# Performance work log

Hardware: AMD Instinct MI355X
Metric: run time of the kernel (lower is better)

## Reference

```python
import jax, jax.numpy as jnp
import numpy as np

N = 500_000      # total observations
D = 40           # per-observation feature dim
S = 2048         # number of segments (time series)
WIDTH = 128      # psi hidden width
LATENT = 128     # latent width
DOT = 64         # dot_prod_dim
HEADS = 4        # n_heads


def setup_inputs() -> dict:
    key = jax.random.key(0)
    ks = jax.random.split(key, 12)

    def he(k, shape):
        fan_in = shape[0]
        lim = np.sqrt(6.0 / fan_in)
        return jax.random.uniform(k, shape, jnp.float32, -lim, lim)

    inputs = jax.random.normal(ks[0], (N, D), jnp.float32)
    segment_ids = jnp.sort(jax.random.randint(ks[1], (N,), 0, S))
    lengths = jax.random.randint(ks[2], (S,), 0, 300)
    return {
        "inputs": inputs,
        "segment_ids": segment_ids,
        "lengths": lengths,
        "W1": he(ks[3], (D, WIDTH)),      "b1": jnp.zeros((WIDTH,), jnp.float32),
        "W2": he(ks[4], (WIDTH, WIDTH)), "b2": jnp.zeros((WIDTH,), jnp.float32),
        "W3": he(ks[5], (WIDTH, LATENT)),"b3": jnp.zeros((LATENT,), jnp.float32),
        "Wr": he(ks[6], (LATENT, LATENT)),"br": jnp.zeros((LATENT,), jnp.float32),
        "W_k": he(ks[7], (LATENT + D, DOT * HEADS)),
        "W_q": jax.random.normal(ks[8], (HEADS, DOT), jnp.float32) * 0.02,
    }


def segment_softmax(x, seg, num_segments):
    # x: [N, H]; softmax over elements sharing the same segment id
    m = jax.ops.segment_max(x, seg, num_segments, indices_are_sorted=True)
    e = jnp.exp(x - m[seg])
    denom = jax.ops.segment_sum(e, seg, num_segments, indices_are_sorted=True)
    return e / denom[seg]


def reference(inputs, segment_ids, lengths, W1, b1, W2, b2, W3, b3, Wr, br, W_k, W_q):
    relu = jax.nn.relu
    # psi: 2 hidden dense layers + latent projection (all relu)
    h = relu(inputs @ W1 + b1)
    h = relu(h @ W2 + b2)
    enc = relu(h @ W3 + b3)                                   # [N, LATENT]
    # segment mean aggregation
    sums = jax.ops.segment_sum(enc, segment_ids, S, indices_are_sorted=True)
    counts = jax.ops.segment_sum(jnp.ones((enc.shape[0], 1), enc.dtype),
                                 segment_ids, S, indices_are_sorted=True)
    agg = sums / jnp.maximum(counts, 1.0)                      # [S, LATENT]
    agg = relu(agg @ Wr + br)                                  # rho
    # broadcast back and combine
    combined = jnp.concatenate([inputs, agg[segment_ids]], axis=-1)  # [N, D+LATENT]
    keys = (combined @ W_k).reshape(-1, HEADS, DOT)            # split+stack == reshape
    preattn = jnp.einsum('nhd,hd->nh', keys, W_q) / jnp.sqrt(jnp.float32(DOT))
    attn = segment_softmax(preattn, segment_ids, S)            # [N, H]
    # match original: list of per-head [N, 1] tensors -> stacked [H, N, 1]
    return jnp.transpose(attn)[..., None]
```

## Files before the change

### kernel.cpp

```cpp
#include <hip/hip_runtime.h>
#include <math.h>


#define NROWS 500000
#define DIM 40
#define NSEG 2048
#define DOTD 64
#define NH 4
#define BLOCK 256

__global__ __launch_bounds__(BLOCK) void prep0_kernel(
    const float* __restrict__ Wk,
    const float* __restrict__ Wq,
    float* __restrict__ denom,
    float* __restrict__ wxg)
{
    const int t = (int)(blockIdx.x * BLOCK + threadIdx.x);
    if (t < NSEG * NH) denom[t] = 0.f;
    if (blockIdx.x == 32 && threadIdx.x < DIM * NH) {
        const int d = (int)threadIdx.x >> 2;
        const int h = (int)threadIdx.x & 3;
        const float* wkp = Wk + d * (NH * DOTD) + h * DOTD;
        const float* wqp = Wq + h * DOTD;
        float acc = 0.f;
        #pragma unroll
        for (int j = 0; j < DOTD; ++j) acc += wkp[j] * wqp[j];
        wxg[threadIdx.x] = acc * 0.125f;
    }
}

__global__ __launch_bounds__(BLOCK) void logits_kernel(
    const float* __restrict__ x,
    const int* __restrict__ seg,
    const float* __restrict__ wxg,
    float4* __restrict__ e4,
    float* __restrict__ denom)
{
    __shared__ float wx[DIM][NH];
    const int tid = (int)threadIdx.x;
    if (tid < DIM * NH) ((float*)wx)[tid] = wxg[tid];
    __syncthreads();

    const int n = (int)(blockIdx.x * BLOCK + tid);
    const bool valid = (n < NROWS);
    const int s = valid ? seg[n] : -1;

    float e[NH] = {0.f, 0.f, 0.f, 0.f};
    if (valid) {
        const float4* xr = (const float4*)(x + (size_t)n * DIM);
        float acc[NH] = {0.f, 0.f, 0.f, 0.f};
        #pragma unroll
        for (int q = 0; q < DIM / 4; ++q) {
            const float4 v = xr[q];
            #pragma unroll
            for (int h = 0; h < NH; ++h) {
                acc[h] += v.x * wx[4 * q + 0][h];
                acc[h] += v.y * wx[4 * q + 1][h];
                acc[h] += v.z * wx[4 * q + 2][h];
                acc[h] += v.w * wx[4 * q + 3][h];
            }
        }
        #pragma unroll
        for (int h = 0; h < NH; ++h) e[h] = __expf(acc[h]);
        float4 ev;
        ev.x = e[0]; ev.y = e[1]; ev.z = e[2]; ev.w = e[3];
        e4[n] = ev;
    }

    const int lane = tid & 63;
    const int snext = __shfl_down(s, 1, 64);
    const bool tail = (lane == 63) || (snext != s);

    float v[NH] = {e[0], e[1], e[2], e[3]};
    #pragma unroll
    for (int off = 1; off <= 32; off <<= 1) {
        const int su = __shfl_up(s, off, 64);
        #pragma unroll
        for (int h = 0; h < NH; ++h) {
            const float u = __shfl_up(v[h], off, 64);
            if (lane >= off && su == s) v[h] += u;
        }
    }
    if (tail && valid) {
        #pragma unroll
        for (int h = 0; h < NH; ++h) atomicAdd(&denom[s * NH + h], v[h]);
    }
}

__global__ __launch_bounds__(BLOCK) void norm_kernel(
    const int* __restrict__ seg,
    const float4* __restrict__ e4,
    const float* __restrict__ denom,
    float* __restrict__ out)
{
    const int n = (int)(blockIdx.x * BLOCK + threadIdx.x);
    if (n >= NROWS) return;
    const int s = seg[n];
    const float4 e = e4[n];
    const float4 d = *(const float4*)(denom + s * NH);
    out[(size_t)0 * NROWS + n] = e.x / d.x;
    out[(size_t)1 * NROWS + n] = e.y / d.y;
    out[(size_t)2 * NROWS + n] = e.z / d.z;
    out[(size_t)3 * NROWS + n] = e.w / d.w;
}

extern "C" void kernel_launch(void* const* d_in, const int* in_sizes, int n_in,
                              void* d_out, int out_size, void* d_ws, size_t ws_size,
                              hipStream_t stream) {
    const float* x  = (const float*)d_in[0];
    const int* seg  = (const int*)d_in[1];
    const float* Wk = (const float*)d_in[11];
    const float* Wq = (const float*)d_in[12];
    float* out = (float*)d_out;

    float* denom = (float*)d_ws;
    float* wxg   = denom + NSEG * NH;
    float4* e4   = (float4*)((char*)d_ws + 65536);

    const int rowblocks = (NROWS + BLOCK - 1) / BLOCK;
    hipLaunchKernelGGL(prep0_kernel, dim3(33), dim3(BLOCK), 0, stream,
                       Wk, Wq, denom, wxg);
    hipLaunchKernelGGL(logits_kernel, dim3(rowblocks), dim3(BLOCK), 0, stream,
                       x, seg, wxg, e4, denom);
    hipLaunchKernelGGL(norm_kernel, dim3(rowblocks), dim3(BLOCK), 0, stream,
                       seg, e4, denom, out);
}
```

Before: 148.9 us.

## Fuse softmax into one segment-per-block kernel with wave-level boundary search

Replaces the three-kernel pipeline (prep, logits with atomics, normalize) with one kernel. Each block owns two segments, finds their row ranges with a ballot-based lower-bound search over the sorted ids, keeps exp values in registers, and reduces denominators within the block, so no atomics or intermediate buffer are needed. This removes the e4 round trip through global memory and two launches. Segments longer than the register slices recompute logits in a second pass, and parallelism is limited to 1024 blocks with uneven segment sizes.

Result: slower. 172.1 us (+15.5%).

```diff
diff --git a/kernel.cpp b/kernel.cpp
--- a/kernel.cpp
+++ b/kernel.cpp
@@ -8,100 +8,177 @@
 #define DOTD 64
 #define NH 4
 #define BLOCK 256
+#define SEGB 2
+#define GRID (NSEG / SEGB)
+#define MAXSLICE 3
 
-__global__ __launch_bounds__(BLOCK) void prep0_kernel(
+typedef float v2f __attribute__((ext_vector_type(2)));
+
+__device__ __forceinline__ int wave_lower_bound(const int* __restrict__ seg,
+                                                int target, int lane) {
+    if (target <= 0) return 0;
+    if (target >= NSEG) return NROWS;
+    const int g = (int)(((long long)target * NROWS) >> 11);
+    int idx = g - 2048 + 64 * lane;
+    int c = idx < 0 ? 0 : (idx >= NROWS ? NROWS - 1 : idx);
+    bool pred = (idx < 0) || (idx < NROWS && seg[c] < target);
+    const int t1 = (int)__popcll(__ballot(pred));
+    const int base = g - 2048 + 64 * (t1 - 1) + 1;
+    idx = base + lane;
+    c = idx < 0 ? 0 : (idx >= NROWS ? NROWS - 1 : idx);
+    pred = (idx < 0) || (idx < NROWS && seg[c] < target);
+    int res = base + (int)__popcll(__ballot(pred));
+    bool ok = (res >= 0) && (res <= NROWS);
+    if (ok && res > 0) ok = (seg[res - 1] < target);
+    if (ok && res < NROWS) ok = ok && (seg[res] >= target);
+    if (!ok) {
+        int lo = 0, hi = NROWS;
+        while (lo < hi) { int mid = (lo + hi) >> 1; if (seg[mid] < target) lo = mid + 1; else hi = mid; }
+        res = lo;
+    }
+    return res;
+}
+
+__global__ __launch_bounds__(BLOCK) void fused_kernel(
+    const float* __restrict__ x,
+    const int* __restrict__ seg,
     const float* __restrict__ Wk,
     const float* __restrict__ Wq,
-    float* __restrict__ denom,
-    float* __restrict__ wxg)
+    float* __restrict__ out)
 {
-    const int t = (int)(blockIdx.x * BLOCK + threadIdx.x);
-    if (t < NSEG * NH) denom[t] = 0.f;
-    if (blockIdx.x == 32 && threadIdx.x < DIM * NH) {
-        const int d = (int)threadIdx.x >> 2;
-        const int h = (int)threadIdx.x & 3;
+    __shared__ float wxs[DIM][NH];
+    __shared__ int bnd[SEGB + 1];
+    __shared__ float psum[BLOCK / 64][NH];
+
+    const int tid = (int)threadIdx.x;
+    const int lane = tid & 63;
+    const int wave = tid >> 6;
+
+    if (tid < DIM * NH) {
+        const int d = tid >> 2;
+        const int h = tid & 3;
         const float* wkp = Wk + d * (NH * DOTD) + h * DOTD;
         const float* wqp = Wq + h * DOTD;
         float acc = 0.f;
         #pragma unroll
         for (int j = 0; j < DOTD; ++j) acc += wkp[j] * wqp[j];
-        wxg[threadIdx.x] = acc * 0.125f;
+        wxs[d][h] = acc * 0.125f;
     }
-}
-
-__global__ __launch_bounds__(BLOCK) void logits_kernel(
-    const float* __restrict__ x,
-    const int* __restrict__ seg,
-    const float* __restrict__ wxg,
-    float4* __restrict__ e4,
-    float* __restrict__ denom)
-{
-    __shared__ float wx[DIM][NH];
-    const int tid = (int)threadIdx.x;
-    if (tid < DIM * NH) ((float*)wx)[tid] = wxg[tid];
+    if (wave <= SEGB) {
+        const int b = wave_lower_bound(seg, (int)blockIdx.x * SEGB + wave, lane);
+        if (lane == 0) bnd[wave] = b;
+    }
     __syncthreads();
 
-    const int n = (int)(blockIdx.x * BLOCK + tid);
-    const bool valid = (n < NROWS);
-    const int s = valid ? seg[n] : -1;
+    const int sp = wave >> 1;
+    const int u  = wave & 1;
+    const int start = bnd[sp];
+    const int rows  = bnd[sp + 1] - start;
 
-    float e[NH] = {0.f, 0.f, 0.f, 0.f};
-    if (valid) {
-        const float4* xr = (const float4*)(x + (size_t)n * DIM);
-        float acc[NH] = {0.f, 0.f, 0.f, 0.f};
+    float4 e[MAXSLICE];
+    int r[MAXSLICE];
+    bool val[MAXSLICE];
+    #pragma unroll
+    for (int t = 0; t < MAXSLICE; ++t) { r[t] = 64 * (u + 2 * t) + lane; val[t] = false; }
+    float s0 = 0.f, s1 = 0.f, s2 = 0.f, s3 = 0.f;
+
+    if (rows > 0) {
+        const float* xbase = x + (size_t)start * DIM;
+        #pragma unroll
+        for (int t = 0; t < MAXSLICE; ++t) val[t] = (r[t] < rows);
+        v2f a01[MAXSLICE], a23[MAXSLICE];
+        #pragma unroll
+        for (int t = 0; t < MAXSLICE; ++t) { a01[t] = (v2f){0.f, 0.f}; a23[t] = (v2f){0.f, 0.f}; }
         #pragma unroll
         for (int q = 0; q < DIM / 4; ++q) {
-            const float4 v = xr[q];
+            float4 cch[MAXSLICE];
             #pragma unroll
-            for (int h = 0; h < NH; ++h) {
-                acc[h] += v.x * wx[4 * q + 0][h];
-                acc[h] += v.y * wx[4 * q + 1][h];
-                acc[h] += v.z * wx[4 * q + 2][h];
-                acc[h] += v.w * wx[4 * q + 3][h];
+            for (int t = 0; t < MAXSLICE; ++t) {
+                cch[t] = val[t] ? *(const float4*)(xbase + (size_t)r[t] * DIM + 4 * q)
+                                : make_float4(0.f, 0.f, 0.f, 0.f);
+            }
+            #pragma unroll
+            for (int d = 0; d < 4; ++d) {
+                const v2f w01 = *(const v2f*)&wxs[4 * q + d][0];
+                const v2f w23 = *(const v2f*)&wxs[4 * q + d][2];
+                #pragma unroll
+                for (int t = 0; t < MAXSLICE; ++t) {
+                    const float xv = ((const float*)&cch[t])[d];
+                    const v2f xs = {xv, xv};
+                    a01[t] = __builtin_elementwise_fma(xs, w01, a01[t]);
+                    a23[t] = __builtin_elementwise_fma(xs, w23, a23[t]);
+                }
             }
         }
         #pragma unroll
-        for (int h = 0; h < NH; ++h) e[h] = __expf(acc[h]);
-        float4 ev;
-        ev.x = e[0]; ev.y = e[1]; ev.z = e[2]; ev.w = e[3];
-        e4[n] = ev;
+        for (int t = 0; t < MAXSLICE; ++t) {
+            float4 ev;
+            ev.x = __expf(a01[t][0]); ev.y = __expf(a01[t][1]);
+            ev.z = __expf(a23[t][0]); ev.w = __expf(a23[t][1]);
+            if (!val[t]) ev = make_float4(0.f, 0.f, 0.f, 0.f);
+            e[t] = ev;
+            s0 += ev.x; s1 += ev.y; s2 += ev.z; s3 += ev.w;
+        }
+        for (int k = u + 2 * MAXSLICE; 64 * k < rows; k += 2) {
+            const int rr = 64 * k + lane;
+            if (rr < rows) {
+                const float* xr = xbase + (size_t)rr * DIM;
+                float a[4] = {0.f, 0.f, 0.f, 0.f};
+                for (int dd = 0; dd < DIM; ++dd) {
+                    const float xv = xr[dd];
+                    a[0] += xv * wxs[dd][0]; a[1] += xv * wxs[dd][1];
+                    a[2] += xv * wxs[dd][2]; a[3] += xv * wxs[dd][3];
+                }
+                s0 += __expf(a[0]); s1 += __expf(a[1]);
+                s2 += __expf(a[2]); s3 += __expf(a[3]);
+            }
+        }
     }
 
-    const int lane = tid & 63;
-    const int snext = __shfl_down(s, 1, 64);
-    const bool tail = (lane == 63) || (snext != s);
+    #pragma unroll
+    for (int off = 32; off > 0; off >>= 1) {
+        s0 += __shfl_xor(s0, off, 64); s1 += __shfl_xor(s1, off, 64);
+        s2 += __shfl_xor(s2, off, 64); s3 += __shfl_xor(s3, off, 64);
+    }
+    if (lane == 0) {
+        psum[wave][0] = s0; psum[wave][1] = s1; psum[wave][2] = s2; psum[wave][3] = s3;
+    }
+    __syncthreads();
 
-    float v[NH] = {e[0], e[1], e[2], e[3]};
-    #pragma unroll
-    for (int off = 1; off <= 32; off <<= 1) {
-        const int su = __shfl_up(s, off, 64);
+    if (rows > 0) {
+        const int pw = wave ^ 1;
+        const float rd0 = 1.0f / (s0 + psum[pw][0]);
+        const float rd1 = 1.0f / (s1 + psum[pw][1]);
+        const float rd2 = 1.0f / (s2 + psum[pw][2]);
+        const float rd3 = 1.0f / (s3 + psum[pw][3]);
         #pragma unroll
-        for (int h = 0; h < NH; ++h) {
-            const float u = __shfl_up(v[h], off, 64);
-            if (lane >= off && su == s) v[h] += u;
+        for (int t = 0; t < MAXSLICE; ++t) {
+            if (val[t]) {
+                const int n = start + r[t];
+                out[n] = e[t].x * rd0;
+                out[NROWS + n] = e[t].y * rd1;
+                out[2 * NROWS + n] = e[t].z * rd2;
+                out[3 * NROWS + n] = e[t].w * rd3;
+            }
+        }
+        for (int k = u + 2 * MAXSLICE; 64 * k < rows; k += 2) {
+            const int rr = 64 * k + lane;
+            if (rr < rows) {
+                const float* xr = x + (size_t)(start + rr) * DIM;
+                float a[4] = {0.f, 0.f, 0.f, 0.f};
+                for (int dd = 0; dd < DIM; ++dd) {
+                    const float xv = xr[dd];
+                    a[0] += xv * wxs[dd][0]; a[1] += xv * wxs[dd][1];
+                    a[2] += xv * wxs[dd][2]; a[3] += xv * wxs[dd][3];
+                }
+                const int n = start + rr;
+                out[n] = __expf(a[0]) * rd0;
+                out[NROWS + n] = __expf(a[1]) * rd1;
+                out[2 * NROWS + n] = __expf(a[2]) * rd2;
+                out[3 * NROWS + n] = __expf(a[3]) * rd3;
+            }
         }
     }
-    if (tail && valid) {
-        #pragma unroll
-        for (int h = 0; h < NH; ++h) atomicAdd(&denom[s * NH + h], v[h]);
-    }
-}
-
-__global__ __launch_bounds__(BLOCK) void norm_kernel(
-    const int* __restrict__ seg,
-    const float4* __restrict__ e4,
-    const float* __restrict__ denom,
-    float* __restrict__ out)
-{
-    const int n = (int)(blockIdx.x * BLOCK + threadIdx.x);
-    if (n >= NROWS) return;
-    const int s = seg[n];
-    const float4 e = e4[n];
-    const float4 d = *(const float4*)(denom + s * NH);
-    out[(size_t)0 * NROWS + n] = e.x / d.x;
-    out[(size_t)1 * NROWS + n] = e.y / d.y;
-    out[(size_t)2 * NROWS + n] = e.z / d.z;
-    out[(size_t)3 * NROWS + n] = e.w / d.w;
 }
 
 extern "C" void kernel_launch(void* const* d_in, const int* in_sizes, int n_in,
@@ -112,16 +189,6 @@
     const float* Wk = (const float*)d_in[11];
     const float* Wq = (const float*)d_in[12];
     float* out = (float*)d_out;
-
-    float* denom = (float*)d_ws;
-    float* wxg   = denom + NSEG * NH;
-    float4* e4   = (float4*)((char*)d_ws + 65536);
-
-    const int rowblocks = (NROWS + BLOCK - 1) / BLOCK;
-    hipLaunchKernelGGL(prep0_kernel, dim3(33), dim3(BLOCK), 0, stream,
-                       Wk, Wq, denom, wxg);
-    hipLaunchKernelGGL(logits_kernel, dim3(rowblocks), dim3(BLOCK), 0, stream,
-                       x, seg, wxg, e4, denom);
-    hipLaunchKernelGGL(norm_kernel, dim3(rowblocks), dim3(BLOCK), 0, stream,
-                       seg, e4, denom, out);
+    hipLaunchKernelGGL(fused_kernel, dim3(GRID), dim3(BLOCK), 0, stream,
+                       x, seg, Wk, Wq, out);
 }
```
